# Optimization experiments

Hardware: AMD Instinct MI355X
Metric: run time of the kernel (lower is better)

## Reference

```python
import jax, jax.numpy as jnp
import numpy as np

B, T, C = 4, 2048, 1024
H = 16
HD = C // H  # 64


def setup_inputs() -> dict:
    key = jax.random.key(0)
    k1, k2, k3 = jax.random.split(key, 3)
    x = jax.random.normal(k1, (B, T, C), dtype=jnp.float32)
    W_qkv = jax.random.normal(k2, (3 * C, C), dtype=jnp.float32) * (C ** -0.5)
    W_proj = jax.random.normal(k3, (C, C), dtype=jnp.float32) * (C ** -0.5)
    b_proj = jnp.zeros((C,), dtype=jnp.float32)
    return {"x": x, "W_qkv": W_qkv, "W_proj": W_proj, "b_proj": b_proj}


def reference(x, W_qkv, W_proj, b_proj):
    # qkv = x @ W_qkv.T : [B,T,3C]
    qkv = jnp.einsum('btc,oc->bto', x, W_qkv)
    # Faithful to torch: view(B,T,H,3*HD) then chunk last dim -> per-head q/k/v
    qkv = qkv.reshape(B, T, H, 3 * HD)
    q, k, v = jnp.split(qkv, 3, axis=-1)      # each [B,T,H,HD]
    q = q.transpose(0, 2, 1, 3)               # [B,H,T,HD]
    k = k.transpose(0, 2, 1, 3)
    v = v.transpose(0, 2, 1, 3)
    scale = HD ** -0.5
    att = jnp.einsum('bhqd,bhkd->bhqk', q, k) * scale  # [B,H,T,T]
    causal = jnp.tril(jnp.ones((T, T), dtype=bool))
    att = jnp.where(causal, att, -jnp.inf)
    att = jax.nn.softmax(att, axis=-1)
    out = jnp.einsum('bhqk,bhkd->bhqd', att, v)        # [B,H,T,HD]
    out = out.transpose(0, 2, 1, 3).reshape(B, T, C)
    out = jnp.einsum('btc,oc->bto', out, W_proj) + b_proj
    return out
```

## Files before the change

kernel.cpp:

```cpp
#include <hip/hip_runtime.h>
#include <stdint.h>

#define B_ 4
#define T_ 2048
#define C_ 1024
#define H_ 16
#define HD_ 64

typedef __attribute__((ext_vector_type(8))) short short8;
typedef __attribute__((ext_vector_type(4))) float f32x4;

typedef uint32_t __attribute__((address_space(3))) lds_u32;
typedef const uint32_t __attribute__((address_space(1))) glb_u32;

__device__ inline void async16(const void* g, void* l) {
    __builtin_amdgcn_global_load_lds((glb_u32*)g, (lds_u32*)l, 16, 0, 0);
}

__device__ inline short f2bf(float f) {
    union { float f; uint32_t u; } x; x.f = f;
    uint32_t r = (x.u + 0x7fffu + ((x.u >> 16) & 1u)) >> 16;
    return (short)r;
}
__device__ inline float bf2f(short b) {
    union { uint32_t u; float f; } x; x.u = ((uint32_t)(uint16_t)b) << 16;
    return x.f;
}
__device__ inline uint32_t cvt_pk_bf16(float lo, float hi) {
    uint32_t r;
    asm("v_cvt_pk_bf16_f32 %0, %1, %2" : "=v"(r) : "v"(lo), "v"(hi));
    return r;
}

__global__ void convert_all(const void* __restrict__ x,  const void* __restrict__ wq,
                            const void* __restrict__ wp, const void* __restrict__ bias,
                            short* __restrict__ xd, short* __restrict__ wqd,
                            short* __restrict__ wpd, short* __restrict__ biasd,
                            int* __restrict__ flag_out)
{
    __shared__ int cnt;
    if (threadIdx.x == 0) cnt = 0;
    __syncthreads();
    int sane = 0;
    const uint32_t* xu = (const uint32_t*)x;
    for (int i = threadIdx.x; i < 1024; i += 256) {
        float v = bf2f((short)(xu[i] & 0xFFFFu));
        float a = fabsf(v);
        if (a > 1e-5f && a < 1e5f) sane++;
    }
    atomicAdd(&cnt, sane);
    __syncthreads();
    const int isf32 = (cnt < 512) ? 1 : 0;

    const int blk = blockIdx.x;
    const void* src; short* dst; int base, n;
    if (blk < 4096)      { src = x;    dst = xd;    base = blk;        n = B_*T_*C_; }
    else if (blk < 5632) { src = wq;   dst = wqd;   base = blk - 4096; n = 3*C_*C_; }
    else if (blk < 6144) { src = wp;   dst = wpd;   base = blk - 5632; n = C_*C_; }
    else                 { src = bias; dst = biasd; base = 0;          n = C_;
                           if (threadIdx.x == 0) *flag_out = isf32; }
    const int i = (base * 256 + threadIdx.x) * 8;
    if (i >= n) return;
    if (isf32) {
        const float* s = (const float*)src;
        short8 o;
#pragma unroll
        for (int j = 0; j < 8; j++) o[j] = f2bf(s[i + j]);
        *(short8*)&dst[i] = o;
    } else {
        *(short8*)&dst[i] = *(const short8*)((const short*)src + i);
    }
}

template <bool DUAL>
__global__ __launch_bounds__(256) void gemm_bt(
    const short* __restrict__ A, const short* __restrict__ Bm,
    const short* __restrict__ bias_bf, void* __restrict__ Cout,
    int M, int N, int K, const int* __restrict__ flag)
{
    __shared__ short As[128 * 32];
    __shared__ short Bs[128 * 32];
    const int tid  = threadIdx.x;
    const int lane = tid & 63;
    const int wave = tid >> 6;
    const int quad = lane >> 4;
    const int lcol = lane & 15;
    const int m0 = blockIdx.y * 128;
    const int n0 = blockIdx.x * 128;
    const int wm = (wave >> 1) * 64;
    const int wn = (wave & 1) * 64;
    const int isf32 = DUAL ? *flag : 0;

    f32x4 acc[4][4];
#pragma unroll
    for (int i = 0; i < 4; i++)
#pragma unroll
        for (int j = 0; j < 4; j++) acc[i][j] = f32x4{0.f, 0.f, 0.f, 0.f};

    const int idx0 = tid * 8;
    const int row0 = idx0 >> 5, col0 = idx0 & 31;
    const int idx1 = (256 + tid) * 8;
    const int row1 = idx1 >> 5, col1 = idx1 & 31;

    for (int k0 = 0; k0 < K; k0 += 32) {
        async16(&A[(size_t)(m0 + row0) * K + k0 + col0], &As[idx0]);
        async16(&A[(size_t)(m0 + row1) * K + k0 + col1], &As[idx1]);
        async16(&Bm[(size_t)(n0 + row0) * K + k0 + col0], &Bs[idx0]);
        async16(&Bm[(size_t)(n0 + row1) * K + k0 + col1], &Bs[idx1]);
        __syncthreads();

        short8 af[4], bfr[4];
#pragma unroll
        for (int mi = 0; mi < 4; mi++)
            af[mi] = *(const short8*)&As[(wm + mi * 16 + lcol) * 32 + quad * 8];
#pragma unroll
        for (int ni = 0; ni < 4; ni++)
            bfr[ni] = *(const short8*)&Bs[(wn + ni * 16 + lcol) * 32 + quad * 8];
#pragma unroll
        for (int mi = 0; mi < 4; mi++)
#pragma unroll
            for (int ni = 0; ni < 4; ni++)
                acc[mi][ni] = __builtin_amdgcn_mfma_f32_16x16x32_bf16(
                    af[mi], bfr[ni], acc[mi][ni], 0, 0, 0);
        __syncthreads();
    }

#pragma unroll
    for (int ni = 0; ni < 4; ni++) {
        const int col = n0 + wn + ni * 16 + lcol;
        const float bv = bias_bf ? bf2f(bias_bf[col]) : 0.f;
#pragma unroll
        for (int mi = 0; mi < 4; mi++) {
            const int row = m0 + wm + mi * 16 + quad * 4;
#pragma unroll
            for (int r = 0; r < 4; r++) {
                const float val = acc[mi][ni][r] + bv;
                const size_t off = (size_t)(row + r) * N + col;
                if (DUAL && isf32) ((float*)Cout)[off] = val;
                else               ((short*)Cout)[off] = f2bf(val);
            }
        }
    }
}

__global__ __launch_bounds__(256) void attn(const short* __restrict__ qkv,
                                            short* __restrict__ att)
{
    __shared__ short lds_k[64][72];
    __shared__ short lds_vt[64][68];

    const int tid  = threadIdx.x;
    const int lane = tid & 63;
    const int wave = tid >> 6;
    const int quad = lane >> 4;
    const int lcol = lane & 15;

    const int bh   = blockIdx.x & 63;
    const int j    = blockIdx.x >> 6;
    const int b    = bh >> 4;
    const int h    = bh & 15;

    const size_t rowstride = 3 * C_;
    const size_t bhbase = (size_t)b * T_ * rowstride + (size_t)h * (3 * HD_);

    const int kkey = tid >> 2;
    const int kdp  = (tid & 3) * 16;
    const int vkey = tid & 63;
    const int vkp  = (vkey & 0x23) | ((vkey & 0x0C) << 1) | ((vkey & 0x10) >> 2);
    const int vd0  = (tid >> 6) * 16;

    short8 vones;
#pragma unroll
    for (int i = 0; i < 8; i++) vones[i] = (short)0x3F80;

    const short* kp; const short* vp;
    short8 kA, kB, vA, vB;
    const size_t TILE_STEP = (size_t)64 * rowstride;
    auto load_init = [&]() {
        kp = &qkv[bhbase + (size_t)kkey * rowstride + HD_ + kdp];
        vp = &qkv[bhbase + (size_t)vkey * rowstride + 2 * HD_ + vd0];
    };
    auto load_tile = [&]() {
        kA = *(const short8*)kp;
        kB = *(const short8*)(kp + 8);
        vA = *(const short8*)vp;
        vB = *(const short8*)(vp + 8);
        kp += TILE_STEP; vp += TILE_STEP;
    };

    const float SC = 0.1803368801f;
    auto scale_frag = [&](short8 q) {
        short8 r;
#pragma unroll
        for (int i = 0; i < 8; i++) r[i] = f2bf(bf2f(q[i]) * SC);
        return r;
    };

    auto process_chunk = [&](int qblk, bool sync_first) {
        const int q0 = qblk * 128;
        const int qA = q0 + wave * 16;
        const int qB = q0 + 64 + wave * 16;

        short8 qfA0, qfA1, qfB0, qfB1;
        {
            const size_t ba = bhbase + (size_t)(qA + lcol) * rowstride + quad * 8;
            qfA0 = scale_frag(*(const short8*)&qkv[ba]);
            qfA1 = scale_frag(*(const short8*)&qkv[ba + 32]);
            const size_t bb = bhbase + (size_t)(qB + lcol) * rowstride + quad * 8;
            qfB0 = scale_frag(*(const short8*)&qkv[bb]);
            qfB1 = scale_frag(*(const short8*)&qkv[bb + 32]);
        }

        f32x4 oA[4], oB[4], oLA, oLB;
#pragma unroll
        for (int i = 0; i < 4; i++) { oA[i] = f32x4{0.f,0.f,0.f,0.f}; oB[i] = f32x4{0.f,0.f,0.f,0.f}; }
        oLA = f32x4{0.f,0.f,0.f,0.f}; oLB = f32x4{0.f,0.f,0.f,0.f};

        load_init();
        load_tile();

        const int LT = 2 * qblk + 1;
        for (int kt = 0; kt <= LT; ++kt) {
            if (kt || sync_first) __syncthreads();
            *(short8*)&lds_k[kkey][kdp]     = kA;
            *(short8*)&lds_k[kkey][kdp + 8] = kB;
#pragma unroll
            for (int jj = 0; jj < 8; jj++) {
                lds_vt[vd0 + jj][vkp]     = vA[jj];
                lds_vt[vd0 + 8 + jj][vkp] = vB[jj];
            }
            __syncthreads();
            if (kt < LT) load_tile();

            const int k0 = kt * 64;
            const bool doA = (kt < LT);

            f32x4 SA[4], SB[4];
#pragma unroll
            for (int t = 0; t < 4; t++) {
                const short8 kf0 = *(const short8*)&lds_k[t * 16 + lcol][quad * 8];
                const short8 kf1 = *(const short8*)&lds_k[t * 16 + lcol][32 + quad * 8];
                SB[t] = f32x4{0.f, 0.f, 0.f, 0.f};
                SB[t] = __builtin_amdgcn_mfma_f32_16x16x32_bf16(kf0, qfB0, SB[t], 0, 0, 0);
                SB[t] = __builtin_amdgcn_mfma_f32_16x16x32_bf16(kf1, qfB1, SB[t], 0, 0, 0);
                if (doA) {
                    SA[t] = f32x4{0.f, 0.f, 0.f, 0.f};
                    SA[t] = __builtin_amdgcn_mfma_f32_16x16x32_bf16(kf0, qfA0, SA[t], 0, 0, 0);
                    SA[t] = __builtin_amdgcn_mfma_f32_16x16x32_bf16(kf1, qfA1, SA[t], 0, 0, 0);
                }
            }

            short8 vf[4][2];
#pragma unroll
            for (int dt = 0; dt < 4; dt++) {
                vf[dt][0] = *(const short8*)&lds_vt[dt * 16 + lcol][quad * 8];
                vf[dt][1] = *(const short8*)&lds_vt[dt * 16 + lcol][32 + quad * 8];
            }

            auto do_mtile = [&](f32x4 (&S)[4], f32x4 (&o)[4], f32x4& oL,
                                int qX, bool maskT) {
                if (maskT) {
                    const int qthr = qX + lcol - k0 - quad * 4;
#pragma unroll
                    for (int t = 0; t < 4; t++)
#pragma unroll
                        for (int r = 0; r < 4; r++) {
                            float e = __builtin_amdgcn_exp2f(S[t][r]);
                            if (t * 16 + r > qthr) e = 0.f;
                            S[t][r] = e;
                        }
                } else {
#pragma unroll
                    for (int t = 0; t < 4; t++)
#pragma unroll
                        for (int r = 0; r < 4; r++)
                            S[t][r] = __builtin_amdgcn_exp2f(S[t][r]);
                }
                union { uint32_t u[4]; short8 s; } p0, p1;
#pragma unroll
                for (int w = 0; w < 4; w++) {
                    const int t0 = w >> 1, r0 = (w & 1) * 2;
                    p0.u[w] = cvt_pk_bf16(S[t0][r0],     S[t0][r0 + 1]);
                    p1.u[w] = cvt_pk_bf16(S[2 + t0][r0], S[2 + t0][r0 + 1]);
                }
                oL = __builtin_amdgcn_mfma_f32_16x16x32_bf16(p0.s, vones, oL, 0, 0, 0);
                oL = __builtin_amdgcn_mfma_f32_16x16x32_bf16(p1.s, vones, oL, 0, 0, 0);
#pragma unroll
                for (int dt = 0; dt < 4; dt++) {
                    o[dt] = __builtin_amdgcn_mfma_f32_16x16x32_bf16(p0.s, vf[dt][0], o[dt], 0, 0, 0);
                    o[dt] = __builtin_amdgcn_mfma_f32_16x16x32_bf16(p1.s, vf[dt][1], o[dt], 0, 0, 0);
                }
            };

            if (doA) do_mtile(SA, oA, oLA, qA, kt == LT - 1);
            do_mtile(SB, oB, oLB, qB, kt == LT);
        }

#pragma unroll
        for (int r = 0; r < 4; r++) {
            const float la = oLA[r], lb = oLB[r];
            const float iar = (la > 0.f) ? 1.f / la : 0.f;
            const float ibr = (lb > 0.f) ? 1.f / lb : 0.f;
            const int qi  = quad * 4 + r;
            const int qrA = qA + qi;
            const int qrB = qB + qi;
#pragma unroll
            for (int dt = 0; dt < 4; dt++) {
                const int col = h * HD_ + dt * 16 + lcol;
                att[(size_t)(b * T_ + qrA) * C_ + col] = f2bf(oA[dt][r] * iar);
                att[(size_t)(b * T_ + qrB) * C_ + col] = f2bf(oB[dt][r] * ibr);
            }
        }
    };

    process_chunk(15 - j, false);
    process_chunk(j, true);
}

extern "C" void kernel_launch(void* const* d_in, const int* in_sizes, int n_in,
                              void* d_out, int out_size, void* d_ws, size_t ws_size,
                              hipStream_t stream) {
    char* ws = (char*)d_ws;
    short* qkv     = (short*)(ws);
    short* x_or_at = (short*)(ws + 50331648);
    short* wq_bf   = (short*)(ws + 50331648 + 16777216);
    short* wp_bf   = (short*)(ws + 50331648 + 16777216 + 6291456);
    short* bias_bf = (short*)(ws + 50331648 + 16777216 + 6291456 + 2097152);
    int*   flag    = (int*)  (ws + 50331648 + 16777216 + 6291456 + 2097152 + 2048);

    dim3 blk(256);

    convert_all<<<dim3(6145), blk, 0, stream>>>(
        d_in[0], d_in[1], d_in[2], d_in[3],
        x_or_at, wq_bf, wp_bf, bias_bf, flag);

    gemm_bt<false><<<dim3((3 * C_) / 128, (B_ * T_) / 128), blk, 0, stream>>>(
        x_or_at, wq_bf, nullptr, qkv, B_ * T_, 3 * C_, C_, flag);

    attn<<<dim3(B_ * H_ * (T_ / 256)), blk, 0, stream>>>(qkv, x_or_at);

    gemm_bt<true><<<dim3(C_ / 128, (B_ * T_) / 128), blk, 0, stream>>>(
        x_or_at, wp_bf, bias_bf, d_out, B_ * T_, C_, C_, flag);
}
```

Baseline: 260.5 us.

## Replace GEMM with 256x256 tile, 8-wave double-buffered pipelined kernel

Both GEMMs now use a new kernel with 256x256 output tiles, 512 threads and a K-step of 64. It double-buffers LDS with async global-to-LDS loads interleaved between MFMA phases, and adds XOR-swizzled LDS layouts to avoid bank conflicts. It also remaps block IDs per XCD for L2 locality and raises MFMA priority with setprio. The aim is to hide global load latency and raise arithmetic intensity over the old 128x128 single-buffered loop that synced twice per step. The cost is 128KB of LDS per block and many barriers, and the larger tiles give far fewer blocks (128 for the projection GEMM), which risks poor occupancy.

```diff
diff --git a/kernel.cpp b/kernel.cpp
--- a/kernel.cpp
+++ b/kernel.cpp
@@ -31,6 +31,10 @@
     asm("v_cvt_pk_bf16_f32 %0, %1, %2" : "=v"(r) : "v"(lo), "v"(hi));
     return r;
 }
+
+#define FENCE asm volatile("" ::: "memory")
+#define BAR   do { FENCE; __builtin_amdgcn_s_barrier(); FENCE; } while (0)
+#define VMC4  asm volatile("s_waitcnt vmcnt(4)" ::: "memory")
 
 __global__ void convert_all(const void* __restrict__ x,  const void* __restrict__ wq,
                             const void* __restrict__ wp, const void* __restrict__ bias,
@@ -73,65 +77,126 @@
 }
 
 template <bool DUAL>
-__global__ __launch_bounds__(256) void gemm_bt(
+__global__ __launch_bounds__(512, 2) void gemm8(
     const short* __restrict__ A, const short* __restrict__ Bm,
     const short* __restrict__ bias_bf, void* __restrict__ Cout,
     int M, int N, int K, const int* __restrict__ flag)
 {
-    __shared__ short As[128 * 32];
-    __shared__ short Bs[128 * 32];
+    __shared__ short lds[65536];
     const int tid  = threadIdx.x;
     const int lane = tid & 63;
-    const int wave = tid >> 6;
+    const int wid  = tid >> 6;
     const int quad = lane >> 4;
     const int lcol = lane & 15;
-    const int m0 = blockIdx.y * 128;
-    const int n0 = blockIdx.x * 128;
-    const int wm = (wave >> 1) * 64;
-    const int wn = (wave & 1) * 64;
+    const int wm   = wid >> 2;
+    const int wn   = wid & 3;
+    const int nbx  = N >> 8;
+
+    const int nwg = gridDim.x;
+    const int qq = nwg >> 3, rr = nwg & 7;
+    const int xcd = blockIdx.x & 7, lid = blockIdx.x >> 3;
+    const int wg = (xcd < rr ? xcd * (qq + 1) : rr * (qq + 1) + (xcd - rr) * qq) + lid;
+    const int m0 = (wg / nbx) << 8;
+    const int n0 = (wg % nbx) << 8;
     const int isf32 = DUAL ? *flag : 0;
 
-    f32x4 acc[4][4];
-#pragma unroll
-    for (int i = 0; i < 4; i++)
+    const int srow = tid >> 3;
+    const int sch  = ((tid & 7) ^ (srow & 7)) << 3;
+
+    auto stageA = [&](int buf, int h, int kt) {
+        const short* g = &A[(size_t)(m0 + srow + h * 64) * K + kt * 64 + sch];
+        short* l = &lds[buf * 16384 + h * 8192 + tid * 8];
+        async16(g, l);
+        async16(g + (size_t)128 * K, l + 4096);
+    };
+    auto stageB = [&](int buf, int h, int kt) {
+        const int br = (srow & 31) + ((srow >> 5) << 6) + h * 32;
+        const short* g = &Bm[(size_t)(n0 + br) * K + kt * 64 + sch];
+        short* l = &lds[32768 + buf * 16384 + h * 8192 + tid * 8];
+        async16(g, l);
+        async16(g + (size_t)128 * K, l + 4096);
+    };
+
+    f32x4 acc[8][4];
+#pragma unroll
+    for (int i = 0; i < 8; i++)
 #pragma unroll
         for (int j = 0; j < 4; j++) acc[i][j] = f32x4{0.f, 0.f, 0.f, 0.f};
 
-    const int idx0 = tid * 8;
-    const int row0 = idx0 >> 5, col0 = idx0 & 31;
-    const int idx1 = (256 + tid) * 8;
-    const int row1 = idx1 >> 5, col1 = idx1 & 31;
-
-    for (int k0 = 0; k0 < K; k0 += 32) {
-        async16(&A[(size_t)(m0 + row0) * K + k0 + col0], &As[idx0]);
-        async16(&A[(size_t)(m0 + row1) * K + k0 + col1], &As[idx1]);
-        async16(&Bm[(size_t)(n0 + row0) * K + k0 + col0], &Bs[idx0]);
-        async16(&Bm[(size_t)(n0 + row1) * K + k0 + col1], &Bs[idx1]);
-        __syncthreads();
-
-        short8 af[4], bfr[4];
-#pragma unroll
-        for (int mi = 0; mi < 4; mi++)
-            af[mi] = *(const short8*)&As[(wm + mi * 16 + lcol) * 32 + quad * 8];
-#pragma unroll
-        for (int ni = 0; ni < 4; ni++)
-            bfr[ni] = *(const short8*)&Bs[(wn + ni * 16 + lcol) * 32 + quad * 8];
-#pragma unroll
-        for (int mi = 0; mi < 4; mi++)
-#pragma unroll
-            for (int ni = 0; ni < 4; ni++)
-                acc[mi][ni] = __builtin_amdgcn_mfma_f32_16x16x32_bf16(
-                    af[mi], bfr[ni], acc[mi][ni], 0, 0, 0);
-        __syncthreads();
+    short8 a0[8], a1[8], b0[4], b1[4];
+
+    auto rdA = [&](short8* d, int buf, int qm) {
+#pragma unroll
+        for (int m2 = 0; m2 < 4; m2++)
+#pragma unroll
+            for (int ks = 0; ks < 2; ks++)
+                d[m2 * 2 + ks] = *(const short8*)&lds[buf * 16384 + qm * 8192
+                    + (wm * 64 + m2 * 16 + lcol) * 64
+                    + ((((ks << 2) | quad) ^ (lcol & 7)) << 3)];
+    };
+    auto rdB = [&](short8* d, int buf, int qn) {
+#pragma unroll
+        for (int n2 = 0; n2 < 2; n2++)
+#pragma unroll
+            for (int ks = 0; ks < 2; ks++)
+                d[n2 * 2 + ks] = *(const short8*)&lds[32768 + buf * 16384 + qn * 8192
+                    + (wn * 32 + n2 * 16 + lcol) * 64
+                    + ((((ks << 2) | quad) ^ (lcol & 7)) << 3)];
+    };
+    auto mm = [&](short8* a, short8* b, int qm, int qn) {
+        __builtin_amdgcn_s_setprio(1);
+#pragma unroll
+        for (int m2 = 0; m2 < 4; m2++)
+#pragma unroll
+            for (int n2 = 0; n2 < 2; n2++)
+#pragma unroll
+                for (int ks = 0; ks < 2; ks++)
+                    acc[qm * 4 + m2][qn * 2 + n2] = __builtin_amdgcn_mfma_f32_16x16x32_bf16(
+                        a[m2 * 2 + ks], b[n2 * 2 + ks], acc[qm * 4 + m2][qn * 2 + n2], 0, 0, 0);
+        __builtin_amdgcn_s_setprio(0);
+    };
+
+    const int NT = K >> 6;
+    stageB(0, 0, 0); stageA(0, 0, 0); stageB(0, 1, 0); stageA(0, 1, 0);
+    stageB(1, 0, 1); stageA(1, 0, 1);
+    VMC4;
+    BAR;
+
+    for (int i = 0; i < NT / 2; i++) {
+        const int to = 2 * i + 1;
+        const int t2 = (2 * i + 2 < NT) ? 2 * i + 2 : NT - 1;
+        const int t3 = (2 * i + 3 < NT) ? 2 * i + 3 : NT - 1;
+        rdA(a0, 0, 0); rdB(b0, 0, 0);
+        stageB(1, 1, to);
+        BAR; mm(a0, b0, 0, 0); BAR;
+        rdA(a1, 0, 1);
+        stageA(1, 1, to);
+        BAR; mm(a1, b0, 1, 0); BAR;
+        rdB(b1, 0, 1);
+        stageB(0, 0, t2);
+        BAR; mm(a0, b1, 0, 1); BAR;
+        stageA(0, 0, t2);
+        BAR; mm(a1, b1, 1, 1); VMC4; BAR;
+        rdA(a0, 1, 0); rdB(b0, 1, 0);
+        stageB(0, 1, t2);
+        BAR; mm(a0, b0, 0, 0); BAR;
+        rdA(a1, 1, 1);
+        stageA(0, 1, t2);
+        BAR; mm(a1, b0, 1, 0); BAR;
+        rdB(b1, 1, 1);
+        stageB(1, 0, t3);
+        BAR; mm(a0, b1, 0, 1); BAR;
+        stageA(1, 0, t3);
+        BAR; mm(a1, b1, 1, 1); VMC4; BAR;
     }
 
 #pragma unroll
     for (int ni = 0; ni < 4; ni++) {
-        const int col = n0 + wn + ni * 16 + lcol;
+        const int col = n0 + wn * 64 + ni * 16 + lcol;
         const float bv = bias_bf ? bf2f(bias_bf[col]) : 0.f;
 #pragma unroll
-        for (int mi = 0; mi < 4; mi++) {
-            const int row = m0 + wm + mi * 16 + quad * 4;
+        for (int mi = 0; mi < 8; mi++) {
+            const int row = m0 + wm * 128 + mi * 16 + quad * 4;
 #pragma unroll
             for (int r = 0; r < 4; r++) {
                 const float val = acc[mi][ni][r] + bv;
@@ -334,11 +399,11 @@
         d_in[0], d_in[1], d_in[2], d_in[3],
         x_or_at, wq_bf, wp_bf, bias_bf, flag);
 
-    gemm_bt<false><<<dim3((3 * C_) / 128, (B_ * T_) / 128), blk, 0, stream>>>(
+    gemm8<false><<<dim3(384), dim3(512), 0, stream>>>(
         x_or_at, wq_bf, nullptr, qkv, B_ * T_, 3 * C_, C_, flag);
 
     attn<<<dim3(B_ * H_ * (T_ / 256)), blk, 0, stream>>>(qkv, x_or_at);
 
-    gemm_bt<true><<<dim3(C_ / 128, (B_ * T_) / 128), blk, 0, stream>>>(
+    gemm8<true><<<dim3(128), dim3(512), 0, stream>>>(
         x_or_at, wp_bf, bias_bf, d_out, B_ * T_, C_, C_, flag);
 }
```

New measurement: 253.7 us. -2.6%, faster.
